# Kernel tuning notes

Measured on AMD Instinct MI355X. Metric: run time of the kernel, lower is better.

The kernel has to match this reference:

```python
import jax, jax.numpy as jnp
import numpy as np

EPS = 1e-5

def _proj(x, w, b, gamma, beta, mean, var):
    # 1x1 conv (einsum over channels) + BatchNorm (inference) ; Dropout is identity in eval.
    y = jnp.einsum('bchw,oc->bohw', x, w) + b[None, :, None, None]
    scale = gamma * jax.lax.rsqrt(var + EPS)
    shift = beta - mean * scale
    return y * scale[None, :, None, None] + shift[None, :, None, None]

def _make_layer(key, cin, cout):
    k1, k2, k3, k4 = jax.random.split(key, 4)
    w = jax.random.normal(k1, (cout, cin), jnp.float32) * (1.0 / np.sqrt(cin))
    b = jax.random.normal(k2, (cout,), jnp.float32) * 0.01
    gamma = 1.0 + 0.1 * jax.random.normal(k3, (cout,), jnp.float32)
    beta = 0.1 * jax.random.normal(k4, (cout,), jnp.float32)
    mean = 0.05 * jax.random.normal(jax.random.fold_in(k1, 7), (cout,), jnp.float32)
    var = 0.5 + jax.random.uniform(jax.random.fold_in(k2, 7), (cout,), jnp.float32)
    return w, b, gamma, beta, mean, var

def setup_inputs() -> dict:
    key = jax.random.key(0)
    B, C, Ci, H, W = 4, 128, 64, 64, 64
    ks = jax.random.split(key, 6)
    inp = {
        'x1': jax.random.normal(ks[0], (B, C, H, W), jnp.float32),
        'x2': jax.random.normal(ks[1], (B, C, H, W), jnp.float32),
    }
    for name, k, cin, cout in [('theta', ks[2], C, Ci), ('phi', ks[3], C, Ci),
                               ('g', ks[4], C, Ci), ('wout', ks[5], Ci, C)]:
        w, b, gm, bt, mn, vr = _make_layer(k, cin, cout)
        inp.update({f'{name}_w': w, f'{name}_b': b, f'{name}_g': gm,
                    f'{name}_beta': bt, f'{name}_m': mn, f'{name}_v': vr})
    return inp

def reference(x1, x2,
              theta_w, theta_b, theta_g, theta_beta, theta_m, theta_v,
              phi_w, phi_b, phi_g, phi_beta, phi_m, phi_v,
              g_w, g_b, g_g, g_beta, g_m, g_v,
              wout_w, wout_b, wout_g, wout_beta, wout_m, wout_v):
    B, C, H, W = x1.shape
    N = H * W
    theta_x1 = _proj(x1, theta_w, theta_b, theta_g, theta_beta, theta_m, theta_v).reshape(B, -1, N)  # [B,Ci,N]
    phi_x2 = _proj(x2, phi_w, phi_b, phi_g, phi_beta, phi_m, phi_v).reshape(B, -1, N)                # [B,Ci,N]
    g_x2 = _proj(x2, g_w, g_b, g_g, g_beta, g_m, g_v).reshape(B, -1, N)                              # [B,Ci,N]
    # attention_map[b, n, m] = sum_c theta[b,c,n] * phi[b,c,m]
    attn = jax.nn.softmax(jnp.einsum('bcn,bcm->bnm', theta_x1, phi_x2), axis=-1)  # [B,N,N]
    out = jnp.einsum('bnm,bcm->bcn', attn, g_x2).reshape(B, -1, H, W)             # [B,Ci,H,W]
    out = _proj(out, wout_w, wout_b, wout_g, wout_beta, wout_m, wout_v)           # [B,C,H,W]
    return jnp.concatenate((out, x1), axis=1)                                     # [B,2C,H,W]
```

## Files before the change

### kernel.cpp

```cpp
#include <hip/hip_runtime.h>
#include <stdint.h>
#include <stddef.h>

#define EPS   1e-5f
#define CINCH 128
#define CI    64
#define NPIX  4096

typedef __bf16 bf16_t;
typedef bf16_t bf16x8 __attribute__((ext_vector_type(8)));
typedef float  f32x4  __attribute__((ext_vector_type(4)));

typedef __attribute__((address_space(3))) unsigned int lds_u32;
typedef __attribute__((address_space(1))) const unsigned int glb_u32;

__device__ __forceinline__ f32x4 mfma16(bf16x8 a, bf16x8 b, f32x4 c) {
  return __builtin_amdgcn_mfma_f32_16x16x32_bf16(a, b, c, 0, 0, 0);
}
__device__ __forceinline__ f32x4 fzero4() {
  f32x4 z = {0.f, 0.f, 0.f, 0.f};
  return z;
}
__device__ __forceinline__ void gload16(const void* g, void* l) {
  __builtin_amdgcn_global_load_lds((glb_u32*)g, (lds_u32*)l, 16, 0, 0);
}


__global__ __launch_bounds__(256) void proj_theta(
    const float* __restrict__ x1,
    const float* __restrict__ w,  const float* __restrict__ bb,
    const float* __restrict__ gm, const float* __restrict__ bt,
    const float* __restrict__ mn, const float* __restrict__ vr,
    bf16_t* __restrict__ thetaT_h, bf16_t* __restrict__ thetaT_l,
    float* __restrict__ out)
{
  __shared__ float wT[CINCH][CI];
  __shared__ float bfold[CI];
  __shared__ float tileF[32][68];

  const int tid = threadIdx.x;
  const int b   = blockIdx.y;
  const int n0  = blockIdx.x * 32;

  for (int idx = tid; idx < CI * CINCH; idx += 256) {
    const int o = idx & 63, c = idx >> 6;
    const float sc = gm[o] * rsqrtf(vr[o] + EPS);
    wT[c][o] = w[o * CINCH + c] * sc;
    if (c == 0) bfold[o] = bb[o] * sc + bt[o] - mn[o] * sc;
  }
  __syncthreads();

  const int px = tid & 31;
  const int og = tid >> 5;
  const float* xb = x1 + (size_t)b * CINCH * NPIX + n0 + px;

  float acc[8];
#pragma unroll
  for (int j = 0; j < 8; ++j) acc[j] = 0.f;

#pragma unroll 4
  for (int c0 = 0; c0 < CINCH; c0 += 4) {
    float xv[4];
#pragma unroll
    for (int cc = 0; cc < 4; ++cc) xv[cc] = xb[(size_t)(c0 + cc) * NPIX];
#pragma unroll
    for (int cc = 0; cc < 4; ++cc) {
      const f32x4 w0 = *(const f32x4*)&wT[c0 + cc][og * 8];
      const f32x4 w1 = *(const f32x4*)&wT[c0 + cc][og * 8 + 4];
#pragma unroll
      for (int j = 0; j < 4; ++j) {
        acc[j]     += w0[j] * xv[cc];
        acc[j + 4] += w1[j] * xv[cc];
      }
    }
  }
#pragma unroll
  for (int j = 0; j < 8; ++j) tileF[px][og * 8 + j] = acc[j] + bfold[og * 8 + j];
  __syncthreads();

  {
    const int px2 = tid >> 3, ogs = tid & 7;
    bf16x8 hv, lv;
#pragma unroll
    for (int j = 0; j < 8; ++j) {
      const float v = tileF[px2][ogs * 8 + j];
      const bf16_t h = (bf16_t)v;
      hv[j] = h;
      lv[j] = (bf16_t)(v - (float)h);
    }
    const size_t base = ((size_t)b * NPIX + n0 + px2) * CI + ogs * 8;
    *(bf16x8*)(thetaT_h + base) = hv;
    *(bf16x8*)(thetaT_l + base) = lv;
  }

#pragma unroll
  for (int i = 0; i < 4; ++i) {
    const int idx = i * 256 + tid;
    const int c = idx >> 3, n4 = (idx & 7) * 4;
    *(f32x4*)(out + ((size_t)b * 256 + 128 + c) * NPIX + n0 + n4) =
        *(const f32x4*)(x1 + ((size_t)b * CINCH + c) * NPIX + n0 + n4);
  }
}

__global__ __launch_bounds__(256) void proj_phi(
    const float* __restrict__ x2,
    const float* __restrict__ w,  const float* __restrict__ bb,
    const float* __restrict__ gm, const float* __restrict__ bt,
    const float* __restrict__ mn, const float* __restrict__ vr,
    bf16_t* __restrict__ phiT_h, bf16_t* __restrict__ phiT_l)
{
  __shared__ float wT[CINCH][CI];
  __shared__ float bfold[CI];
  __shared__ float tileF[32][68];

  const int tid = threadIdx.x;
  const int b   = blockIdx.y;
  const int n0  = blockIdx.x * 32;

  for (int idx = tid; idx < CI * CINCH; idx += 256) {
    const int o = idx & 63, c = idx >> 6;
    const float sc = gm[o] * rsqrtf(vr[o] + EPS);
    wT[c][o] = w[o * CINCH + c] * sc;
    if (c == 0) bfold[o] = bb[o] * sc + bt[o] - mn[o] * sc;
  }
  __syncthreads();

  const int px = tid & 31;
  const int og = tid >> 5;
  const float* xb = x2 + (size_t)b * CINCH * NPIX + n0 + px;

  float acc[8];
#pragma unroll
  for (int j = 0; j < 8; ++j) acc[j] = 0.f;

#pragma unroll 4
  for (int c0 = 0; c0 < CINCH; c0 += 4) {
    float xv[4];
#pragma unroll
    for (int cc = 0; cc < 4; ++cc) xv[cc] = xb[(size_t)(c0 + cc) * NPIX];
#pragma unroll
    for (int cc = 0; cc < 4; ++cc) {
      const f32x4 w0 = *(const f32x4*)&wT[c0 + cc][og * 8];
      const f32x4 w1 = *(const f32x4*)&wT[c0 + cc][og * 8 + 4];
#pragma unroll
      for (int j = 0; j < 4; ++j) {
        acc[j]     += w0[j] * xv[cc];
        acc[j + 4] += w1[j] * xv[cc];
      }
    }
  }
#pragma unroll
  for (int j = 0; j < 8; ++j) tileF[px][og * 8 + j] = acc[j] + bfold[og * 8 + j];
  __syncthreads();

  {
    const int px2 = tid >> 3, ogs = tid & 7;
    const int n = n0 + px2;
    bf16x8 hv, lv;
#pragma unroll
    for (int j = 0; j < 8; ++j) {
      const float v = tileF[px2][ogs * 8 + j];
      const bf16_t h = (bf16_t)v;
      hv[j] = h;
      lv[j] = (bf16_t)(v - (float)h);
    }
    const size_t rowb = ((size_t)b * NPIX + n) * 128;
    const int byte = (ogs * 16) ^ ((n & 7) << 4);
    *(bf16x8*)((char*)phiT_h + rowb + byte) = hv;
    *(bf16x8*)((char*)phiT_l + rowb + byte) = lv;
  }
}

__global__ __launch_bounds__(256) void proj_g(
    const float* __restrict__ x2,
    const float* __restrict__ w,  const float* __restrict__ bb,
    const float* __restrict__ gm, const float* __restrict__ bt,
    const float* __restrict__ mn, const float* __restrict__ vr,
    bf16_t* __restrict__ g_cm)
{
  __shared__ float wT[CINCH][CI];
  __shared__ float bfold[CI];
  __shared__ float gT[CI][33];

  const int tid = threadIdx.x;
  const int b   = blockIdx.y;
  const int n0  = blockIdx.x * 32;

  for (int idx = tid; idx < CI * CINCH; idx += 256) {
    const int o = idx & 63, c = idx >> 6;
    const float sc = gm[o] * rsqrtf(vr[o] + EPS);
    wT[c][o] = w[o * CINCH + c] * sc;
    if (c == 0) bfold[o] = bb[o] * sc + bt[o] - mn[o] * sc;
  }
  __syncthreads();

  const int px = tid & 31;
  const int og = tid >> 5;
  const float* xb = x2 + (size_t)b * CINCH * NPIX + n0 + px;

  float acc[8];
#pragma unroll
  for (int j = 0; j < 8; ++j) acc[j] = 0.f;

#pragma unroll 4
  for (int c0 = 0; c0 < CINCH; c0 += 4) {
    float xv[4];
#pragma unroll
    for (int cc = 0; cc < 4; ++cc) xv[cc] = xb[(size_t)(c0 + cc) * NPIX];
#pragma unroll
    for (int cc = 0; cc < 4; ++cc) {
      const f32x4 w0 = *(const f32x4*)&wT[c0 + cc][og * 8];
      const f32x4 w1 = *(const f32x4*)&wT[c0 + cc][og * 8 + 4];
#pragma unroll
      for (int j = 0; j < 4; ++j) {
        acc[j]     += w0[j] * xv[cc];
        acc[j + 4] += w1[j] * xv[cc];
      }
    }
  }
#pragma unroll
  for (int j = 0; j < 8; ++j) gT[og * 8 + j][px] = acc[j] + bfold[og * 8 + j];
  __syncthreads();

  {
    const int c  = tid & 63;
    const int mgp = tid >> 6;
    bf16x8 gv;
#pragma unroll
    for (int j = 0; j < 8; ++j) gv[j] = (bf16_t)gT[c][mgp * 8 + j];
    const int m = n0 + mgp * 8;
    char* rowc = (char*)g_cm + ((size_t)b * CI + c) * (NPIX * 2);
    const int byte = ((m & ~63) * 2) + ((((m & 63) * 2) ^ ((c & 7) << 4)));
    *(bf16x8*)(rowc + byte) = gv;
  }
}

__global__ __launch_bounds__(256, 2) void flash_attn(
    const bf16_t* __restrict__ thetaT_h, const bf16_t* __restrict__ thetaT_l,
    const bf16_t* __restrict__ phiT_h,   const bf16_t* __restrict__ phiT_l,
    const bf16_t* __restrict__ g_cm,
    float* __restrict__ Opart, float* __restrict__ mlbuf)
{
  __shared__ __attribute__((aligned(16))) char sTile[2][24576];
  __shared__ __attribute__((aligned(16))) char sP[4][32 * 144];

  const int tid  = threadIdx.x;
  const int lane = tid & 63;
  const int wid  = tid >> 6;
  const int lrow = lane & 15;
  const int lhi  = lane >> 4;

  const int wg = blockIdx.x;
  const int b  = wg >> 7;
  const int qt = (wg & 127) >> 2;
  const int ks = wg & 3;
  const int q0 = qt * 128 + wid * 32;
  const int m0 = ks * 1024;

  const char* const srcPHb = (const char*)phiT_h + ((size_t)b * NPIX) * 128;
  const char* const srcPLb = (const char*)phiT_l + ((size_t)b * NPIX) * 128;
  const char* const srcVb  = (const char*)g_cm + (size_t)b * CI * (NPIX * 2);

  auto stage = [&](int buf, int kb) {
    const int mg = m0 + kb * 64;
    const char* srcPH = srcPHb + (size_t)mg * 128;
    const char* srcPL = srcPLb + (size_t)mg * 128;
    const char* srcV  = srcVb + (size_t)mg * 2;
    char* const dst = sTile[buf];
    int c;
    c = tid;       gload16(srcPH + c * 16, dst + c * 16);
    c = 256 + tid; gload16(srcPH + c * 16, dst + c * 16);
    c = tid;       gload16(srcPL + c * 16, dst + 8192 + c * 16);
    c = 256 + tid; gload16(srcPL + c * 16, dst + 8192 + c * 16);
    c = tid;       gload16(srcV + (size_t)(c >> 3) * (NPIX * 2) + (c & 7) * 16,
                           dst + 16384 + c * 16);
    c = 256 + tid; gload16(srcV + (size_t)(c >> 3) * (NPIX * 2) + (c & 7) * 16,
                           dst + 16384 + c * 16);
  };

  bf16x8 qh[2][2], qlv[2][2];
  {
    const bf16_t* qbh = thetaT_h + ((size_t)b * NPIX + q0 + lrow) * CI + lhi * 8;
    const bf16_t* qbl = thetaT_l + ((size_t)b * NPIX + q0 + lrow) * CI + lhi * 8;
#pragma unroll
    for (int nt = 0; nt < 2; ++nt)
#pragma unroll
      for (int kk = 0; kk < 2; ++kk) {
        qh[nt][kk]  = *(const bf16x8*)(qbh + nt * 16 * CI + kk * 32);
        qlv[nt][kk] = *(const bf16x8*)(qbl + nt * 16 * CI + kk * 32);
      }
  }

  f32x4 oacc[2][4];
#pragma unroll
  for (int a = 0; a < 2; ++a)
#pragma unroll
    for (int c = 0; c < 4; ++c) oacc[a][c] = fzero4();

  float m_run[2] = {-1e30f, -1e30f};
  float l_run[2] = {0.f, 0.f};

  char* const Pw = sP[wid];

  stage(0, 0);
  __syncthreads();

  for (int kb = 0; kb < 16; ++kb) {
    const int cur = kb & 1;
    if (kb < 15) stage(cur ^ 1, kb + 1);

    const char* const sPhiH = sTile[cur];
    const char* const sPhiL = sTile[cur] + 8192;
    const char* const sV    = sTile[cur] + 16384;

    f32x4 s[4][2];
#pragma unroll
    for (int mt = 0; mt < 4; ++mt)
#pragma unroll
      for (int nt = 0; nt < 2; ++nt) s[mt][nt] = fzero4();

#pragma unroll
    for (int mt = 0; mt < 4; ++mt) {
      const int row = mt * 16 + lrow;
      const int swz = (row & 7) << 4;
#pragma unroll
      for (int kk = 0; kk < 2; ++kk) {
        const int byte = row * 128 + ((kk * 64 + lhi * 16) ^ swz);
        const bf16x8 aH = *(const bf16x8*)(sPhiH + byte);
        const bf16x8 aL = *(const bf16x8*)(sPhiL + byte);
#pragma unroll
        for (int nt = 0; nt < 2; ++nt) {
          s[mt][nt] = mfma16(aH, qh[nt][kk],  s[mt][nt]);
          s[mt][nt] = mfma16(aH, qlv[nt][kk], s[mt][nt]);
          s[mt][nt] = mfma16(aL, qh[nt][kk],  s[mt][nt]);
        }
      }
    }

    float a2[2];
#pragma unroll
    for (int nt = 0; nt < 2; ++nt) {
      float mx = -1e30f;
#pragma unroll
      for (int mt = 0; mt < 4; ++mt)
#pragma unroll
        for (int r = 0; r < 4; ++r) mx = fmaxf(mx, s[mt][nt][r]);
      mx = fmaxf(mx, __shfl_xor(mx, 16));
      mx = fmaxf(mx, __shfl_xor(mx, 32));
      const float mnew  = fmaxf(m_run[nt], mx);
      const float alpha = __expf(m_run[nt] - mnew);
      float lsum = 0.f;
#pragma unroll
      for (int mt = 0; mt < 4; ++mt)
#pragma unroll
        for (int r = 0; r < 4; ++r) {
          const float p = __expf(s[mt][nt][r] - mnew);
          s[mt][nt][r] = p;
          lsum += p;
        }
      lsum += __shfl_xor(lsum, 16);
      lsum += __shfl_xor(lsum, 32);
      l_run[nt] = l_run[nt] * alpha + lsum;
      m_run[nt] = mnew;
      a2[nt] = alpha;
    }

#pragma unroll
    for (int qt2 = 0; qt2 < 2; ++qt2) {
#pragma unroll
      for (int r = 0; r < 4; ++r) {
        const float av = __shfl(a2[qt2], lhi * 4 + r);
#pragma unroll
        for (int ct = 0; ct < 4; ++ct) oacc[qt2][ct][r] *= av;
      }
    }

#pragma unroll
    for (int mt = 0; mt < 4; ++mt)
#pragma unroll
      for (int nt = 0; nt < 2; ++nt) {
        union { bf16_t h[4]; uint32_t u[2]; } pk;
#pragma unroll
        for (int r = 0; r < 4; ++r) pk.h[r] = (bf16_t)s[mt][nt][r];
        const int q    = nt * 16 + lrow;
        const int mloc = mt * 16 + lhi * 4;
        *(uint2*)(Pw + q * 144 + mloc * 2) = make_uint2(pk.u[0], pk.u[1]);
      }

    bf16x8 bV[2][4];
#pragma unroll
    for (int ct = 0; ct < 4; ++ct) {
      const int row = ct * 16 + lrow;
      const int swz = (row & 7) << 4;
#pragma unroll
      for (int kk = 0; kk < 2; ++kk)
        bV[kk][ct] = *(const bf16x8*)(sV + row * 128 + ((kk * 64 + lhi * 16) ^ swz));
    }
#pragma unroll
    for (int qt2 = 0; qt2 < 2; ++qt2) {
#pragma unroll
      for (int kk = 0; kk < 2; ++kk) {
        const bf16x8 pfrag =
            *(const bf16x8*)(Pw + (qt2 * 16 + lrow) * 144 + kk * 64 + lhi * 16);
#pragma unroll
        for (int ct = 0; ct < 4; ++ct)
          oacc[qt2][ct] = mfma16(pfrag, bV[kk][ct], oacc[qt2][ct]);
      }
    }

    if (kb < 15) __syncthreads();
  }

#pragma unroll
  for (int qt2 = 0; qt2 < 2; ++qt2)
#pragma unroll
    for (int ct = 0; ct < 4; ++ct)
#pragma unroll
      for (int r = 0; r < 4; ++r) {
        const int q = q0 + qt2 * 16 + lhi * 4 + r;
        const int c = ct * 16 + lrow;
        Opart[(((size_t)b * NPIX + q) * 4 + ks) * 64 + c] = oacc[qt2][ct][r];
      }
  if (lhi < 2) {
    const int q = q0 + lhi * 16 + lrow;
    const size_t base = (((size_t)b * NPIX + q) * 4 + ks) * 2;
    mlbuf[base]     = m_run[lhi];
    mlbuf[base + 1] = l_run[lhi];
  }
}

__global__ __launch_bounds__(256) void merge_out(
    const float* __restrict__ Opart, const float* __restrict__ mlbuf,
    const float* __restrict__ ww,  const float* __restrict__ wb,
    const float* __restrict__ wg,  const float* __restrict__ wbt,
    const float* __restrict__ wm,  const float* __restrict__ wvv,
    float* __restrict__ out)
{
  __shared__ float wlds[128][64];
  __shared__ float bfw[128];
  __shared__ float mrg[32][68];

  const int tid = threadIdx.x;
  const int b   = blockIdx.y;
  const int n0  = blockIdx.x * 32;

  for (int idx = tid; idx < 128 * 64; idx += 256) {
    const int o = idx >> 6, c = idx & 63;
    const float sc = wg[o] * rsqrtf(wvv[o] + EPS);
    wlds[o][c] = ww[o * 64 + c] * sc;
    if (c == 0) bfw[o] = wb[o] * sc + wbt[o] - wm[o] * sc;
  }

  {
    const int px = tid & 31;
    const int cg = tid >> 5;
    const int q  = n0 + px;
    const size_t sb = ((size_t)b * NPIX + q) * 4;
    float mk[4], lk[4];
#pragma unroll
    for (int ks = 0; ks < 4; ++ks) {
      mk[ks] = mlbuf[(sb + ks) * 2];
      lk[ks] = mlbuf[(sb + ks) * 2 + 1];
    }
    const float M = fmaxf(fmaxf(mk[0], mk[1]), fmaxf(mk[2], mk[3]));
    float al[4]; float den = 0.f;
#pragma unroll
    for (int ks = 0; ks < 4; ++ks) { al[ks] = __expf(mk[ks] - M); den += al[ks] * lk[ks]; }
    const float inv = 1.f / den;
#pragma unroll
    for (int ks = 0; ks < 4; ++ks) al[ks] *= inv;

    f32x4 r0 = fzero4(), r1 = fzero4();
#pragma unroll
    for (int ks = 0; ks < 4; ++ks) {
      const f32x4 p0 = *(const f32x4*)(Opart + (sb + ks) * 64 + cg * 8);
      const f32x4 p1 = *(const f32x4*)(Opart + (sb + ks) * 64 + cg * 8 + 4);
      r0 += p0 * al[ks];
      r1 += p1 * al[ks];
    }
    *(f32x4*)&mrg[px][cg * 8]     = r0;
    *(f32x4*)&mrg[px][cg * 8 + 4] = r1;
  }
  __syncthreads();

  const int px = tid & 31;
  const int oh = tid >> 5;
  float acc[16];
#pragma unroll
  for (int j = 0; j < 16; ++j) acc[j] = 0.f;

#pragma unroll 4
  for (int c0 = 0; c0 < 64; c0 += 4) {
    const f32x4 m4 = *(const f32x4*)&mrg[px][c0];
#pragma unroll
    for (int j = 0; j < 16; ++j) {
      const f32x4 w4 = *(const f32x4*)&wlds[oh * 16 + j][c0];
      acc[j] += w4[0] * m4[0] + w4[1] * m4[1] + w4[2] * m4[2] + w4[3] * m4[3];
    }
  }
#pragma unroll
  for (int j = 0; j < 16; ++j) {
    const int o = oh * 16 + j;
    out[((size_t)b * 256 + o) * NPIX + n0 + px] = acc[j] + bfw[o];
  }
}

extern "C" void kernel_launch(void* const* d_in, const int* in_sizes, int n_in,
                              void* d_out, int out_size, void* d_ws, size_t ws_size,
                              hipStream_t stream) {
  (void)in_sizes; (void)n_in; (void)out_size; (void)ws_size;
  const float* x1  = (const float*)d_in[0];
  const float* x2  = (const float*)d_in[1];
  const float* tw  = (const float*)d_in[2];
  const float* tb  = (const float*)d_in[3];
  const float* tg  = (const float*)d_in[4];
  const float* tbt = (const float*)d_in[5];
  const float* tm  = (const float*)d_in[6];
  const float* tv  = (const float*)d_in[7];
  const float* pw  = (const float*)d_in[8];
  const float* pb  = (const float*)d_in[9];
  const float* pg  = (const float*)d_in[10];
  const float* pbt = (const float*)d_in[11];
  const float* pm  = (const float*)d_in[12];
  const float* pv  = (const float*)d_in[13];
  const float* gw  = (const float*)d_in[14];
  const float* gb  = (const float*)d_in[15];
  const float* gg  = (const float*)d_in[16];
  const float* gbt = (const float*)d_in[17];
  const float* gmn = (const float*)d_in[18];
  const float* gv  = (const float*)d_in[19];
  const float* ww  = (const float*)d_in[20];
  const float* wb  = (const float*)d_in[21];
  const float* wg  = (const float*)d_in[22];
  const float* wbt = (const float*)d_in[23];
  const float* wm  = (const float*)d_in[24];
  const float* wv  = (const float*)d_in[25];

  float* out = (float*)d_out;
  char*  ws  = (char*)d_ws;
  bf16_t* thetaT_h = (bf16_t*)(ws);
  bf16_t* thetaT_l = (bf16_t*)(ws + (size_t)(2)  * 1048576);
  bf16_t* phiT_h   = (bf16_t*)(ws + (size_t)(4)  * 1048576);
  bf16_t* phiT_l   = (bf16_t*)(ws + (size_t)(6)  * 1048576);
  bf16_t* g_cm     = (bf16_t*)(ws + (size_t)(8)  * 1048576);
  float*  Opart    = (float*) (ws + (size_t)(10) * 1048576);
  float*  mlbuf    = (float*) (ws + (size_t)(26) * 1048576);

  dim3 gp(128, 4);
  proj_theta<<<gp, 256, 0, stream>>>(x1, tw, tb, tg, tbt, tm, tv,
                                     thetaT_h, thetaT_l, out);
  proj_phi<<<gp, 256, 0, stream>>>(x2, pw, pb, pg, pbt, pm, pv,
                                   phiT_h, phiT_l);
  proj_g<<<gp, 256, 0, stream>>>(x2, gw, gb, gg, gbt, gmn, gv, g_cm);
  flash_attn<<<512, 256, 0, stream>>>(thetaT_h, thetaT_l, phiT_h, phiT_l,
                                      g_cm, Opart, mlbuf);
  merge_out<<<gp, 256, 0, stream>>>(Opart, mlbuf, ww, wb, wg, wbt, wm, wv, out);
}
```

Before: 238.3 us.

## Retile flash attention to 32-key blocks, 6-way key split, fp16 partials, exp2

Splits the key dimension six ways instead of four, giving 768 workgroups, and raises the occupancy hint to three blocks per CU. Key tiles shrink from 64 to 32 rows, and V is now staged through registers into padded LDS instead of swizzled async loads. The log2(e) factor is folded into the theta projection so the softmax can use exp2. Partial outputs are stored as fp16 to halve merge traffic, and the MFMA sections are bracketed with setprio. The trade-offs are more per-tile synchronisation, a larger merge step, and some precision loss in the partials.

New measurement: 238.3 us. No clear change (+0.0%).

```diff
diff --git a/kernel.cpp b/kernel.cpp
--- a/kernel.cpp
+++ b/kernel.cpp
@@ -6,9 +6,13 @@
 #define CINCH 128
 #define CI    64
 #define NPIX  4096
+#define KSPL  6
+#define LOG2E 1.44269504088896340736f
 
 typedef __bf16 bf16_t;
+typedef _Float16 f16_t;
 typedef bf16_t bf16x8 __attribute__((ext_vector_type(8)));
+typedef f16_t  f16x8  __attribute__((ext_vector_type(8)));
 typedef float  f32x4  __attribute__((ext_vector_type(4)));
 
 typedef __attribute__((address_space(3))) unsigned int lds_u32;
@@ -45,8 +49,8 @@
   for (int idx = tid; idx < CI * CINCH; idx += 256) {
     const int o = idx & 63, c = idx >> 6;
     const float sc = gm[o] * rsqrtf(vr[o] + EPS);
-    wT[c][o] = w[o * CINCH + c] * sc;
-    if (c == 0) bfold[o] = bb[o] * sc + bt[o] - mn[o] * sc;
+    wT[c][o] = w[o * CINCH + c] * sc * LOG2E;
+    if (c == 0) bfold[o] = (bb[o] * sc + bt[o] - mn[o] * sc) * LOG2E;
   }
   __syncthreads();
 
@@ -223,26 +227,23 @@
   __syncthreads();
 
   {
-    const int c  = tid & 63;
-    const int mgp = tid >> 6;
+    const int c = tid & 63, mgp = tid >> 6;
     bf16x8 gv;
 #pragma unroll
     for (int j = 0; j < 8; ++j) gv[j] = (bf16_t)gT[c][mgp * 8 + j];
-    const int m = n0 + mgp * 8;
-    char* rowc = (char*)g_cm + ((size_t)b * CI + c) * (NPIX * 2);
-    const int byte = ((m & ~63) * 2) + ((((m & 63) * 2) ^ ((c & 7) << 4)));
-    *(bf16x8*)(rowc + byte) = gv;
-  }
-}
-
-__global__ __launch_bounds__(256, 2) void flash_attn(
+    *(bf16x8*)(g_cm + ((size_t)b * CI + c) * NPIX + n0 + mgp * 8) = gv;
+  }
+}
+
+__global__ __launch_bounds__(256, 3) void flash_attn(
     const bf16_t* __restrict__ thetaT_h, const bf16_t* __restrict__ thetaT_l,
     const bf16_t* __restrict__ phiT_h,   const bf16_t* __restrict__ phiT_l,
     const bf16_t* __restrict__ g_cm,
-    float* __restrict__ Opart, float* __restrict__ mlbuf)
+    f16_t* __restrict__ Opart, float* __restrict__ mlbuf)
 {
-  __shared__ __attribute__((aligned(16))) char sTile[2][24576];
-  __shared__ __attribute__((aligned(16))) char sP[4][32 * 144];
+  __shared__ __attribute__((aligned(16))) char sK[2][8192];
+  __shared__ __attribute__((aligned(16))) char sV[2][64 * 80];
+  __shared__ __attribute__((aligned(16))) char sP[4][32 * 80];
 
   const int tid  = threadIdx.x;
   const int lane = tid & 63;
@@ -251,31 +252,30 @@
   const int lhi  = lane >> 4;
 
   const int wg = blockIdx.x;
-  const int b  = wg >> 7;
-  const int qt = (wg & 127) >> 2;
-  const int ks = wg & 3;
+  const int b  = wg / 192;
+  const int rr = wg % 192;
+  const int qt = rr / KSPL;
+  const int ks = rr % KSPL;
   const int q0 = qt * 128 + wid * 32;
-  const int m0 = ks * 1024;
+  const int t0 = (ks * 128) / KSPL;
+  const int t1 = ((ks + 1) * 128) / KSPL;
 
   const char* const srcPHb = (const char*)phiT_h + ((size_t)b * NPIX) * 128;
   const char* const srcPLb = (const char*)phiT_l + ((size_t)b * NPIX) * 128;
-  const char* const srcVb  = (const char*)g_cm + (size_t)b * CI * (NPIX * 2);
-
-  auto stage = [&](int buf, int kb) {
-    const int mg = m0 + kb * 64;
-    const char* srcPH = srcPHb + (size_t)mg * 128;
-    const char* srcPL = srcPLb + (size_t)mg * 128;
-    const char* srcV  = srcVb + (size_t)mg * 2;
-    char* const dst = sTile[buf];
-    int c;
-    c = tid;       gload16(srcPH + c * 16, dst + c * 16);
-    c = 256 + tid; gload16(srcPH + c * 16, dst + c * 16);
-    c = tid;       gload16(srcPL + c * 16, dst + 8192 + c * 16);
-    c = 256 + tid; gload16(srcPL + c * 16, dst + 8192 + c * 16);
-    c = tid;       gload16(srcV + (size_t)(c >> 3) * (NPIX * 2) + (c & 7) * 16,
-                           dst + 16384 + c * 16);
-    c = 256 + tid; gload16(srcV + (size_t)(c >> 3) * (NPIX * 2) + (c & 7) * 16,
-                           dst + 16384 + c * 16);
+  const char* const srcVb  = (const char*)g_cm + (size_t)b * CI * NPIX * 2;
+
+  const int vc = tid >> 2, vp = tid & 3;
+
+  auto stageK = [&](int buf, int tile) {
+    const size_t rb = (size_t)tile * 32 * 128;
+    gload16(srcPHb + rb + tid * 16, sK[buf] + tid * 16);
+    gload16(srcPLb + rb + tid * 16, sK[buf] + 4096 + tid * 16);
+  };
+  auto loadV = [&](int tile) {
+    return *(const f32x4*)(srcVb + ((size_t)vc * NPIX + tile * 32 + vp * 8) * 2);
+  };
+  auto writeV = [&](int buf, f32x4 v) {
+    *(f32x4*)(sV[buf] + vc * 80 + vp * 16) = v;
   };
 
   bf16x8 qh[2][2], qlv[2][2];
@@ -302,32 +302,35 @@
 
   char* const Pw = sP[wid];
 
-  stage(0, 0);
-  __syncthreads();
-
-  for (int kb = 0; kb < 16; ++kb) {
-    const int cur = kb & 1;
-    if (kb < 15) stage(cur ^ 1, kb + 1);
-
-    const char* const sPhiH = sTile[cur];
-    const char* const sPhiL = sTile[cur] + 8192;
-    const char* const sV    = sTile[cur] + 16384;
-
-    f32x4 s[4][2];
-#pragma unroll
-    for (int mt = 0; mt < 4; ++mt)
+  stageK(0, t0);
+  writeV(0, loadV(t0));
+  __syncthreads();
+
+  for (int t = t0; t < t1; ++t) {
+    const int cur = (t - t0) & 1;
+    const bool more = (t + 1 < t1);
+    f32x4 vnext;
+    if (more) { stageK(cur ^ 1, t + 1); vnext = loadV(t + 1); }
+
+    const char* const sKH = sK[cur];
+    const char* const sKL = sK[cur] + 4096;
+
+    f32x4 s[2][2];
+#pragma unroll
+    for (int mt = 0; mt < 2; ++mt)
 #pragma unroll
       for (int nt = 0; nt < 2; ++nt) s[mt][nt] = fzero4();
 
-#pragma unroll
-    for (int mt = 0; mt < 4; ++mt) {
+    __builtin_amdgcn_s_setprio(1);
+#pragma unroll
+    for (int mt = 0; mt < 2; ++mt) {
       const int row = mt * 16 + lrow;
       const int swz = (row & 7) << 4;
 #pragma unroll
       for (int kk = 0; kk < 2; ++kk) {
         const int byte = row * 128 + ((kk * 64 + lhi * 16) ^ swz);
-        const bf16x8 aH = *(const bf16x8*)(sPhiH + byte);
-        const bf16x8 aL = *(const bf16x8*)(sPhiL + byte);
+        const bf16x8 aH = *(const bf16x8*)(sKH + byte);
+        const bf16x8 aL = *(const bf16x8*)(sKL + byte);
 #pragma unroll
         for (int nt = 0; nt < 2; ++nt) {
           s[mt][nt] = mfma16(aH, qh[nt][kk],  s[mt][nt]);
@@ -336,25 +339,25 @@
         }
       }
     }
+    __builtin_amdgcn_s_setprio(0);
 
     float a2[2];
 #pragma unroll
     for (int nt = 0; nt < 2; ++nt) {
-      float mx = -1e30f;
-#pragma unroll
-      for (int mt = 0; mt < 4; ++mt)
-#pragma unroll
-        for (int r = 0; r < 4; ++r) mx = fmaxf(mx, s[mt][nt][r]);
+      float mx = fmaxf(fmaxf(fmaxf(s[0][nt][0], s[0][nt][1]),
+                             fmaxf(s[0][nt][2], s[0][nt][3])),
+                       fmaxf(fmaxf(s[1][nt][0], s[1][nt][1]),
+                             fmaxf(s[1][nt][2], s[1][nt][3])));
       mx = fmaxf(mx, __shfl_xor(mx, 16));
       mx = fmaxf(mx, __shfl_xor(mx, 32));
       const float mnew  = fmaxf(m_run[nt], mx);
-      const float alpha = __expf(m_run[nt] - mnew);
+      const float alpha = exp2f(m_run[nt] - mnew);
       float lsum = 0.f;
 #pragma unroll
-      for (int mt = 0; mt < 4; ++mt)
+      for (int mt = 0; mt < 2; ++mt)
 #pragma unroll
         for (int r = 0; r < 4; ++r) {
-          const float p = __expf(s[mt][nt][r] - mnew);
+          const float p = exp2f(s[mt][nt][r] - mnew);
           s[mt][nt][r] = p;
           lsum += p;
         }
@@ -376,7 +379,7 @@
     }
 
 #pragma unroll
-    for (int mt = 0; mt < 4; ++mt)
+    for (int mt = 0; mt < 2; ++mt)
 #pragma unroll
       for (int nt = 0; nt < 2; ++nt) {
         union { bf16_t h[4]; uint32_t u[2]; } pk;
@@ -384,33 +387,31 @@
         for (int r = 0; r < 4; ++r) pk.h[r] = (bf16_t)s[mt][nt][r];
         const int q    = nt * 16 + lrow;
         const int mloc = mt * 16 + lhi * 4;
-        *(uint2*)(Pw + q * 144 + mloc * 2) = make_uint2(pk.u[0], pk.u[1]);
-      }
-
-    bf16x8 bV[2][4];
-#pragma unroll
-    for (int ct = 0; ct < 4; ++ct) {
-      const int row = ct * 16 + lrow;
-      const int swz = (row & 7) << 4;
-#pragma unroll
-      for (int kk = 0; kk < 2; ++kk)
-        bV[kk][ct] = *(const bf16x8*)(sV + row * 128 + ((kk * 64 + lhi * 16) ^ swz));
-    }
+        *(uint2*)(Pw + q * 80 + mloc * 2) = make_uint2(pk.u[0], pk.u[1]);
+      }
+
+    if (more) writeV(cur ^ 1, vnext);
+
+    const char* const sVc = sV[cur];
+    bf16x8 bV[4];
+#pragma unroll
+    for (int ct = 0; ct < 4; ++ct)
+      bV[ct] = *(const bf16x8*)(sVc + (ct * 16 + lrow) * 80 + lhi * 16);
+
+    __builtin_amdgcn_s_setprio(1);
 #pragma unroll
     for (int qt2 = 0; qt2 < 2; ++qt2) {
-#pragma unroll
-      for (int kk = 0; kk < 2; ++kk) {
-        const bf16x8 pfrag =
-            *(const bf16x8*)(Pw + (qt2 * 16 + lrow) * 144 + kk * 64 + lhi * 16);
-#pragma unroll
-        for (int ct = 0; ct < 4; ++ct)
-          oacc[qt2][ct] = mfma16(pfrag, bV[kk][ct], oacc[qt2][ct]);
-      }
-    }
-
-    if (kb < 15) __syncthreads();
-  }
-
+      const bf16x8 pfrag = *(const bf16x8*)(Pw + (qt2 * 16 + lrow) * 80 + lhi * 16);
+#pragma unroll
+      for (int ct = 0; ct < 4; ++ct)
+        oacc[qt2][ct] = mfma16(pfrag, bV[ct], oacc[qt2][ct]);
+    }
+    __builtin_amdgcn_s_setprio(0);
+
+    if (more) __syncthreads();
+  }
+
+  f16_t* const Ob = Opart + ((size_t)(b * KSPL + ks) * NPIX) * 64;
 #pragma unroll
   for (int qt2 = 0; qt2 < 2; ++qt2)
 #pragma unroll
@@ -419,18 +420,18 @@
       for (int r = 0; r < 4; ++r) {
         const int q = q0 + qt2 * 16 + lhi * 4 + r;
         const int c = ct * 16 + lrow;
-        Opart[(((size_t)b * NPIX + q) * 4 + ks) * 64 + c] = oacc[qt2][ct][r];
+        Ob[(size_t)q * 64 + c] = (f16_t)oacc[qt2][ct][r];
       }
   if (lhi < 2) {
     const int q = q0 + lhi * 16 + lrow;
-    const size_t base = (((size_t)b * NPIX + q) * 4 + ks) * 2;
+    const size_t base = ((size_t)(b * KSPL + ks) * NPIX + q) * 2;
     mlbuf[base]     = m_run[lhi];
     mlbuf[base + 1] = l_run[lhi];
   }
 }
 
 __global__ __launch_bounds__(256) void merge_out(
-    const float* __restrict__ Opart, const float* __restrict__ mlbuf,
+    const f16_t* __restrict__ Opart, const float* __restrict__ mlbuf,
     const float* __restrict__ ww,  const float* __restrict__ wb,
     const float* __restrict__ wg,  const float* __restrict__ wbt,
     const float* __restrict__ wm,  const float* __restrict__ wvv,
@@ -455,31 +456,35 @@
     const int px = tid & 31;
     const int cg = tid >> 5;
     const int q  = n0 + px;
-    const size_t sb = ((size_t)b * NPIX + q) * 4;
-    float mk[4], lk[4];
-#pragma unroll
-    for (int ks = 0; ks < 4; ++ks) {
-      mk[ks] = mlbuf[(sb + ks) * 2];
-      lk[ks] = mlbuf[(sb + ks) * 2 + 1];
-    }
-    const float M = fmaxf(fmaxf(mk[0], mk[1]), fmaxf(mk[2], mk[3]));
-    float al[4]; float den = 0.f;
-#pragma unroll
-    for (int ks = 0; ks < 4; ++ks) { al[ks] = __expf(mk[ks] - M); den += al[ks] * lk[ks]; }
+    float mk[KSPL], lk[KSPL];
+#pragma unroll
+    for (int ks = 0; ks < KSPL; ++ks) {
+      const size_t base = ((size_t)(b * KSPL + ks) * NPIX + q) * 2;
+      mk[ks] = mlbuf[base];
+      lk[ks] = mlbuf[base + 1];
+    }
+    float M = mk[0];
+#pragma unroll
+    for (int ks = 1; ks < KSPL; ++ks) M = fmaxf(M, mk[ks]);
+    float al[KSPL]; float den = 0.f;
+#pragma unroll
+    for (int ks = 0; ks < KSPL; ++ks) { al[ks] = exp2f(mk[ks] - M); den += al[ks] * lk[ks]; }
     const float inv = 1.f / den;
 #pragma unroll
-    for (int ks = 0; ks < 4; ++ks) al[ks] *= inv;
-
-    f32x4 r0 = fzero4(), r1 = fzero4();
-#pragma unroll
-    for (int ks = 0; ks < 4; ++ks) {
-      const f32x4 p0 = *(const f32x4*)(Opart + (sb + ks) * 64 + cg * 8);
-      const f32x4 p1 = *(const f32x4*)(Opart + (sb + ks) * 64 + cg * 8 + 4);
-      r0 += p0 * al[ks];
-      r1 += p1 * al[ks];
-    }
-    *(f32x4*)&mrg[px][cg * 8]     = r0;
-    *(f32x4*)&mrg[px][cg * 8 + 4] = r1;
+    for (int ks = 0; ks < KSPL; ++ks) al[ks] *= inv;
+
+    float r[8];
+#pragma unroll
+    for (int j = 0; j < 8; ++j) r[j] = 0.f;
+#pragma unroll
+    for (int ks = 0; ks < KSPL; ++ks) {
+      const f16x8 p = *(const f16x8*)(Opart +
+          ((size_t)(b * KSPL + ks) * NPIX + q) * 64 + cg * 8);
+#pragma unroll
+      for (int j = 0; j < 8; ++j) r[j] += (float)p[j] * al[ks];
+    }
+#pragma unroll
+    for (int j = 0; j < 8; ++j) mrg[px][cg * 8 + j] = r[j];
   }
   __syncthreads();
 
@@ -543,8 +548,8 @@
   bf16_t* phiT_h   = (bf16_t*)(ws + (size_t)(4)  * 1048576);
   bf16_t* phiT_l   = (bf16_t*)(ws + (size_t)(6)  * 1048576);
   bf16_t* g_cm     = (bf16_t*)(ws + (size_t)(8)  * 1048576);
-  float*  Opart    = (float*) (ws + (size_t)(10) * 1048576);
-  float*  mlbuf    = (float*) (ws + (size_t)(26) * 1048576);
+  f16_t*  Opart    = (f16_t*) (ws + (size_t)(10) * 1048576);
+  float*  mlbuf    = (float*) (ws + (size_t)(23) * 1048576);
 
   dim3 gp(128, 4);
   proj_theta<<<gp, 256, 0, stream>>>(x1, tw, tb, tg, tbt, tm, tv,
@@ -552,7 +557,7 @@
   proj_phi<<<gp, 256, 0, stream>>>(x2, pw, pb, pg, pbt, pm, pv,
                                    phiT_h, phiT_l);
   proj_g<<<gp, 256, 0, stream>>>(x2, gw, gb, gg, gbt, gmn, gv, g_cm);
-  flash_attn<<<512, 256, 0, stream>>>(thetaT_h, thetaT_l, phiT_h, phiT_l,
+  flash_attn<<<768, 256, 0, stream>>>(thetaT_h, thetaT_l, phiT_h, phiT_l,
                                       g_cm, Opart, mlbuf);
   merge_out<<<gp, 256, 0, stream>>>(Opart, mlbuf, ww, wb, wg, wbt, wm, wv, out);
 }
```
